# Kernel optimization log

Measured on AMD Instinct MI355X. Metric: run time of the kernel, lower is better.

The kernel has to match this reference:

```python
import jax, jax.numpy as jnp
import numpy as np

# Module hyperparameters (from init_kwargs)
MEAN = (0.485, 0.456, 0.406)
STD = (0.229, 0.224, 0.225)
P_ERASE = 0.5
SCALE = (0.02, 0.33)
RATIO = (0.3, 3.3)


def setup_inputs() -> dict:
    key = jax.random.key(0)
    x = jax.random.uniform(key, (64, 3, 384, 384), dtype=jnp.float32)
    mean = jnp.array(MEAN, dtype=jnp.float32).reshape(1, 3, 1, 1)
    std = jnp.array(STD, dtype=jnp.float32).reshape(1, 3, 1, 1)
    return {"x": x, "mean": mean, "std": std}


def reference(x, mean, std):
    """Normalize then apply batched random erasing (training mode).

    Faithful to the torch module, but the per-sample Python loop is replaced
    by a single vectorized mask computation over the whole batch.
    """
    B, C, H, W = x.shape
    xn = (x - mean) / std

    k = jax.random.key(42)
    kp, ka, kr, kt, kl, kn = jax.random.split(k, 6)

    # Per-sample: keep-or-erase coin flip, target area, aspect ratio.
    apply = jax.random.uniform(kp, (B,)) <= P_ERASE
    area = float(H * W)
    ta = jax.random.uniform(ka, (B,), minval=SCALE[0], maxval=SCALE[1]) * area
    ar = jax.random.uniform(kr, (B,), minval=RATIO[0], maxval=RATIO[1])
    h_e = jnp.round(jnp.sqrt(ta * ar)).astype(jnp.int32)
    w_e = jnp.round(jnp.sqrt(ta / ar)).astype(jnp.int32)
    valid = apply & (h_e < H) & (w_e < W)

    # Uniform integer top/left in [0, H-h_e] / [0, W-w_e] (matches randint high=H-h_e+1).
    top = jnp.floor(jax.random.uniform(kt, (B,)) * (H - h_e + 1).astype(jnp.float32)).astype(jnp.int32)
    left = jnp.floor(jax.random.uniform(kl, (B,)) * (W - w_e + 1).astype(jnp.float32)).astype(jnp.int32)

    rows = jnp.arange(H)[None, :]                       # (1, H)
    cols = jnp.arange(W)[None, :]                       # (1, W)
    rmask = (rows >= top[:, None]) & (rows < (top + h_e)[:, None])    # (B, H)
    cmask = (cols >= left[:, None]) & (cols < (left + w_e)[:, None])  # (B, W)
    mask = valid[:, None, None] & rmask[:, :, None] & cmask[:, None, :]  # (B, H, W)

    noise = jax.random.normal(kn, x.shape, dtype=x.dtype)
    return jnp.where(mask[:, None, :, :], noise, xn)
```

## Files before the change

kernel.cpp:

```cpp
#include <hip/hip_runtime.h>
#include <cstring>
#include <cstdint>
#include <cmath>

#define B_IMG 64
#define C_IMG 3
#define H_IMG 384
#define W_IMG 384
#define N_TOT (B_IMG * C_IMG * H_IMG * W_IMG)
#define N4    (N_TOT / 4)

struct Rect { int t, b, l, r; };
struct Params { Rect rc[B_IMG]; };

__host__ __device__ inline uint32_t rotl32(uint32_t x, uint32_t r) {
  return (x << r) | (x >> (32u - r));
}

__host__ __device__ inline void tf2x32(uint32_t k0, uint32_t k1,
                                       uint32_t x0, uint32_t x1,
                                       uint32_t& o0, uint32_t& o1) {
  const uint32_t ks2 = k0 ^ k1 ^ 0x1BD11BDAu;
  x0 += k0; x1 += k1;
  x0 += x1; x1 = rotl32(x1, 13); x1 ^= x0;
  x0 += x1; x1 = rotl32(x1, 15); x1 ^= x0;
  x0 += x1; x1 = rotl32(x1, 26); x1 ^= x0;
  x0 += x1; x1 = rotl32(x1,  6); x1 ^= x0;
  x0 += k1; x1 += ks2 + 1u;
  x0 += x1; x1 = rotl32(x1, 17); x1 ^= x0;
  x0 += x1; x1 = rotl32(x1, 29); x1 ^= x0;
  x0 += x1; x1 = rotl32(x1, 16); x1 ^= x0;
  x0 += x1; x1 = rotl32(x1, 24); x1 ^= x0;
  x0 += ks2; x1 += k0 + 2u;
  x0 += x1; x1 = rotl32(x1, 13); x1 ^= x0;
  x0 += x1; x1 = rotl32(x1, 15); x1 ^= x0;
  x0 += x1; x1 = rotl32(x1, 26); x1 ^= x0;
  x0 += x1; x1 = rotl32(x1,  6); x1 ^= x0;
  x0 += k0; x1 += k1 + 3u;
  x0 += x1; x1 = rotl32(x1, 17); x1 ^= x0;
  x0 += x1; x1 = rotl32(x1, 29); x1 ^= x0;
  x0 += x1; x1 = rotl32(x1, 16); x1 ^= x0;
  x0 += x1; x1 = rotl32(x1, 24); x1 ^= x0;
  x0 += k1; x1 += ks2 + 4u;
  x0 += x1; x1 = rotl32(x1, 13); x1 ^= x0;
  x0 += x1; x1 = rotl32(x1, 15); x1 ^= x0;
  x0 += x1; x1 = rotl32(x1, 26); x1 ^= x0;
  x0 += x1; x1 = rotl32(x1,  6); x1 ^= x0;
  x0 += ks2; x1 += k0 + 5u;
  o0 = x0; o1 = x1;
}

__host__ __device__ inline float unit_from_bits(uint32_t bits) {
  uint32_t fb = (bits >> 9) | 0x3f800000u;
  float f;
#ifdef __HIP_DEVICE_COMPILE__
  f = __uint_as_float(fb);
#else
  memcpy(&f, &fb, 4);
#endif
  return f - 1.0f;
}

__host__ __device__ inline uint32_t rb_partitionable(uint32_t k0, uint32_t k1, uint32_t idx) {
  uint32_t o0, o1;
  tf2x32(k0, k1, 0u, idx, o0, o1);
  return o0 ^ o1;
}

__device__ inline float noise_val(uint32_t idx, uint32_t kn0, uint32_t kn1) {
  const float LO = -0x1.fffffep-1f;
  uint32_t bits = rb_partitionable(kn0, kn1, idx);
  float f = unit_from_bits(bits);
  float u = __fadd_rn(__fmul_rn(f, 2.0f), LO);
  u = fmaxf(LO, u);
  float t  = __fmul_rn(u, u);
  float wv = -log1pf(-t);
  float p;
  if (wv < 5.0f) {
    float ww = __fadd_rn(wv, -2.5f);
    p = 2.81022636e-08f;
    p = __fadd_rn(__fmul_rn(p, ww),  3.43273939e-07f);
    p = __fadd_rn(__fmul_rn(p, ww), -3.5233877e-06f);
    p = __fadd_rn(__fmul_rn(p, ww), -4.39150654e-06f);
    p = __fadd_rn(__fmul_rn(p, ww),  0.00021858087f);
    p = __fadd_rn(__fmul_rn(p, ww), -0.00125372503f);
    p = __fadd_rn(__fmul_rn(p, ww), -0.00417768164f);
    p = __fadd_rn(__fmul_rn(p, ww),  0.246640727f);
    p = __fadd_rn(__fmul_rn(p, ww),  1.50140941f);
  } else {
    float ww = __fadd_rn(__fsqrt_rn(wv), -3.0f);
    p = -0.000200214257f;
    p = __fadd_rn(__fmul_rn(p, ww),  0.000100950558f);
    p = __fadd_rn(__fmul_rn(p, ww),  0.00134934322f);
    p = __fadd_rn(__fmul_rn(p, ww), -0.00367342844f);
    p = __fadd_rn(__fmul_rn(p, ww),  0.00573950773f);
    p = __fadd_rn(__fmul_rn(p, ww), -0.0076224613f);
    p = __fadd_rn(__fmul_rn(p, ww),  0.00943887047f);
    p = __fadd_rn(__fmul_rn(p, ww),  1.00167406f);
    p = __fadd_rn(__fmul_rn(p, ww),  2.83297682f);
  }
  float r = __fmul_rn(p, u);
  return __fmul_rn(1.41421356237f, r);
}

static void compute_host_params(Params& P, uint32_t& kn0, uint32_t& kn1) {
#pragma clang fp contract(off)
  uint32_t keys[6][2];
  for (uint32_t i = 0; i < 6; i++)
    tf2x32(0u, 42u, 0u, i, keys[i][0], keys[i][1]);
  kn0 = keys[5][0]; kn1 = keys[5][1];

  for (int b = 0; b < B_IMG; b++) {
    float u[5];
    for (int k = 0; k < 5; k++)
      u[k] = unit_from_bits(rb_partitionable(keys[k][0], keys[k][1], (uint32_t)b));

    float up = u[0];
    float da = 0.33f - 0.02f;
    float ua = u[1] * da;  ua = ua + 0.02f;  ua = fmaxf(0.02f, ua);
    float ta = ua * 147456.0f;
    float dr = 3.3f - 0.3f;
    float ur = u[2] * dr;  ur = ur + 0.3f;   ur = fmaxf(0.3f, ur);

    float prod = ta * ur;
    float quot = ta / ur;
    int he = (int)rintf(sqrtf(prod));
    int we = (int)rintf(sqrtf(quot));
    bool valid = (up <= 0.5f) && (he < H_IMG) && (we < W_IMG);

    float th = u[3] * (float)(H_IMG - he + 1);
    float tl = u[4] * (float)(W_IMG - we + 1);
    int top  = (int)floorf(th);
    int left = (int)floorf(tl);

    if (valid) { P.rc[b].t = top;  P.rc[b].b = top + he; P.rc[b].l = left; P.rc[b].r = left + we; }
    else       { P.rc[b].t = 0;    P.rc[b].b = 0;        P.rc[b].l = 0;    P.rc[b].r = 0; }
  }
}

__global__ __launch_bounds__(256) void erase_norm_kernel(
    const float* __restrict__ x, const float* __restrict__ mean,
    const float* __restrict__ stdv, float* __restrict__ out,
    Params P, uint32_t kn0, uint32_t kn1) {
  int i4 = blockIdx.x * 256 + threadIdx.x;
  if (i4 >= N4) return;
  int base = i4 * 4;
  int w    = base % W_IMG;
  int rest = base / W_IMG;
  int h  = rest % H_IMG;
  int bc = rest / H_IMG;
  int c  = bc % C_IMG;
  int b  = bc / C_IMG;

  const float4 v = reinterpret_cast<const float4*>(x)[i4];
  float m  = mean[c];
  float sd = stdv[c];
  float4 o;
  o.x = (v.x - m) / sd;
  o.y = (v.y - m) / sd;
  o.z = (v.z - m) / sd;
  o.w = (v.w - m) / sd;

  Rect rc = P.rc[b];
  if (h >= rc.t && h < rc.b && w < rc.r && (w + 3) >= rc.l) {
    if (w     >= rc.l && w     < rc.r) o.x = noise_val((uint32_t)(base + 0), kn0, kn1);
    if (w + 1 >= rc.l && w + 1 < rc.r) o.y = noise_val((uint32_t)(base + 1), kn0, kn1);
    if (w + 2 >= rc.l && w + 2 < rc.r) o.z = noise_val((uint32_t)(base + 2), kn0, kn1);
    if (w + 3 >= rc.l && w + 3 < rc.r) o.w = noise_val((uint32_t)(base + 3), kn0, kn1);
  }
  reinterpret_cast<float4*>(out)[i4] = o;
}

extern "C" void kernel_launch(void* const* d_in, const int* in_sizes, int n_in,
                              void* d_out, int out_size, void* d_ws, size_t ws_size,
                              hipStream_t stream) {
  const float* x    = (const float*)d_in[0];
  const float* mean = (const float*)d_in[1];
  const float* stdv = (const float*)d_in[2];
  float* out = (float*)d_out;

  Params P;
  uint32_t kn0, kn1;
  compute_host_params(P, kn0, kn1);

  int blocks = (N4 + 255) / 256;
  erase_norm_kernel<<<blocks, 256, 0, stream>>>(x, mean, stdv, out, P, kn0, kn1);
}
```

Baseline: 200.2 us.

## Process four float4 per thread with plane-aligned blocks and nontemporal stores

Each block now covers 4096 floats inside a single channel plane, so channel and batch indices are computed once per block instead of by per-element division. Each thread issues four float4 loads up front to raise memory-level parallelism, replaces the divide by std with an FMA using a reciprocal, and writes output with nontemporal stores to avoid polluting cache. The reciprocal-FMA can differ from the reference by rounding, and there are four times fewer blocks.

```diff
diff --git a/kernel.cpp b/kernel.cpp
--- a/kernel.cpp
+++ b/kernel.cpp
@@ -7,8 +7,13 @@
 #define C_IMG 3
 #define H_IMG 384
 #define W_IMG 384
-#define N_TOT (B_IMG * C_IMG * H_IMG * W_IMG)
+#define PLANE (H_IMG * W_IMG)
+#define N_TOT (B_IMG * C_IMG * PLANE)
 #define N4    (N_TOT / 4)
+#define F_PER_BLOCK 4096
+#define BLOCKS (N_TOT / F_PER_BLOCK)
+
+typedef float nfloat4 __attribute__((ext_vector_type(4)));
 
 struct Rect { int t, b, l, r; };
 struct Params { Rect rc[B_IMG]; };
@@ -122,16 +127,12 @@
     float dr = 3.3f - 0.3f;
     float ur = u[2] * dr;  ur = ur + 0.3f;   ur = fmaxf(0.3f, ur);
 
-    float prod = ta * ur;
-    float quot = ta / ur;
-    int he = (int)rintf(sqrtf(prod));
-    int we = (int)rintf(sqrtf(quot));
+    int he = (int)rintf(sqrtf(ta * ur));
+    int we = (int)rintf(sqrtf(ta / ur));
     bool valid = (up <= 0.5f) && (he < H_IMG) && (we < W_IMG);
 
-    float th = u[3] * (float)(H_IMG - he + 1);
-    float tl = u[4] * (float)(W_IMG - we + 1);
-    int top  = (int)floorf(th);
-    int left = (int)floorf(tl);
+    int top  = (int)floorf(u[3] * (float)(H_IMG - he + 1));
+    int left = (int)floorf(u[4] * (float)(W_IMG - we + 1));
 
     if (valid) { P.rc[b].t = top;  P.rc[b].b = top + he; P.rc[b].l = left; P.rc[b].r = left + we; }
     else       { P.rc[b].t = 0;    P.rc[b].b = 0;        P.rc[b].l = 0;    P.rc[b].r = 0; }
@@ -142,33 +143,48 @@
     const float* __restrict__ x, const float* __restrict__ mean,
     const float* __restrict__ stdv, float* __restrict__ out,
     Params P, uint32_t kn0, uint32_t kn1) {
-  int i4 = blockIdx.x * 256 + threadIdx.x;
-  if (i4 >= N4) return;
-  int base = i4 * 4;
-  int w    = base % W_IMG;
-  int rest = base / W_IMG;
-  int h  = rest % H_IMG;
-  int bc = rest / H_IMG;
-  int c  = bc % C_IMG;
-  int b  = bc / C_IMG;
-
-  const float4 v = reinterpret_cast<const float4*>(x)[i4];
-  float m  = mean[c];
-  float sd = stdv[c];
-  float4 o;
-  o.x = (v.x - m) / sd;
-  o.y = (v.y - m) / sd;
-  o.z = (v.z - m) / sd;
-  o.w = (v.w - m) / sd;
-
-  Rect rc = P.rc[b];
-  if (h >= rc.t && h < rc.b && w < rc.r && (w + 3) >= rc.l) {
-    if (w     >= rc.l && w     < rc.r) o.x = noise_val((uint32_t)(base + 0), kn0, kn1);
-    if (w + 1 >= rc.l && w + 1 < rc.r) o.y = noise_val((uint32_t)(base + 1), kn0, kn1);
-    if (w + 2 >= rc.l && w + 2 < rc.r) o.z = noise_val((uint32_t)(base + 2), kn0, kn1);
-    if (w + 3 >= rc.l && w + 3 < rc.r) o.w = noise_val((uint32_t)(base + 3), kn0, kn1);
-  }
-  reinterpret_cast<float4*>(out)[i4] = o;
+  const int t = threadIdx.x;
+  const int plane = blockIdx.x / (PLANE / F_PER_BLOCK);
+  const int c = plane % C_IMG;
+  const int b = plane / C_IMG;
+
+  const nfloat4* __restrict__ x4 = reinterpret_cast<const nfloat4*>(x);
+  nfloat4* __restrict__ o4 = reinterpret_cast<nfloat4*>(out);
+
+  int i4[4];
+  nfloat4 v[4];
+#pragma unroll
+  for (int j = 0; j < 4; j++) {
+    i4[j] = blockIdx.x * 1024 + j * 256 + t;
+    v[j] = x4[i4[j]];
+  }
+
+  const float m  = mean[c];
+  const float rs = 1.0f / stdv[c];
+  const float nm = -m * rs;
+  const Rect rc = P.rc[b];
+  const int planeBase = plane * PLANE;
+
+#pragma unroll
+  for (int j = 0; j < 4; j++) {
+    nfloat4 o;
+    o.x = fmaf(v[j].x, rs, nm);
+    o.y = fmaf(v[j].y, rs, nm);
+    o.z = fmaf(v[j].z, rs, nm);
+    o.w = fmaf(v[j].w, rs, nm);
+
+    const int base = i4[j] * 4;
+    const int rel  = base - planeBase;
+    const int h = rel / W_IMG;
+    const int w = rel - h * W_IMG;
+    if (h >= rc.t && h < rc.b && w < rc.r && (w + 3) >= rc.l) {
+      if (w     >= rc.l && w     < rc.r) o.x = noise_val((uint32_t)(base + 0), kn0, kn1);
+      if (w + 1 >= rc.l && w + 1 < rc.r) o.y = noise_val((uint32_t)(base + 1), kn0, kn1);
+      if (w + 2 >= rc.l && w + 2 < rc.r) o.z = noise_val((uint32_t)(base + 2), kn0, kn1);
+      if (w + 3 >= rc.l && w + 3 < rc.r) o.w = noise_val((uint32_t)(base + 3), kn0, kn1);
+    }
+    __builtin_nontemporal_store(o, &o4[i4[j]]);
+  }
 }
 
 extern "C" void kernel_launch(void* const* d_in, const int* in_sizes, int n_in,
@@ -183,6 +199,5 @@
   uint32_t kn0, kn1;
   compute_host_params(P, kn0, kn1);
 
-  int blocks = (N4 + 255) / 256;
-  erase_norm_kernel<<<blocks, 256, 0, stream>>>(x, mean, stdv, out, P, kn0, kn1);
-}
+  erase_norm_kernel<<<BLOCKS, 256, 0, stream>>>(x, mean, stdv, out, P, kn0, kn1);
+}
```

Measured after the change: 213.4 us. +6.6%, slower.
